# Optimization experiments

Measured on AMD Instinct MI355X. Metric: run time of the kernel, lower is better.

Reference implementation:

```python
import jax, jax.numpy as jnp
import numpy as np

N, E, G = 30000, 240000, 1000
F, H = 78, 10            # in-features, GAT heads
HID = F * H              # 780
NEG_SLOPE = 0.2


def setup_inputs() -> dict:
    key = jax.random.key(0)
    ks = jax.random.split(key, 12)
    x = jax.random.normal(ks[0], (N, F), dtype=jnp.float32)
    edge_index = jax.random.randint(ks[1], (2, E), 0, N, dtype=jnp.int32)
    batch = jnp.sort(jax.random.randint(ks[2], (N,), 0, G, dtype=jnp.int32))
    def lin(k, fan_in, shape):
        return (jax.random.normal(k, shape, dtype=jnp.float32)
                / jnp.sqrt(jnp.float32(fan_in)))
    return {
        "x": x,
        "edge_index": edge_index,
        "batch": batch,
        "W_gat": lin(ks[3], F, (F, HID)),          # GATConv lin weight
        "att_src": lin(ks[4], F, (H, F)),          # GAT attention vectors
        "att_dst": lin(ks[5], F, (H, F)),
        "b_gat": jnp.zeros((HID,), jnp.float32),
        "W_gcn": lin(ks[6], HID, (HID, HID)),
        "b_gcn": jnp.zeros((HID,), jnp.float32),
        "W1": lin(ks[7], 2 * HID, (2 * HID, 1500)),
        "b1": jnp.zeros((1500,), jnp.float32),
        "W2": lin(ks[8], 1500, (1500, 128)),
        "b2": jnp.zeros((128,), jnp.float32),
    }


def _with_self_loops(edge_index):
    loop = jnp.arange(N, dtype=edge_index.dtype)
    src = jnp.concatenate([edge_index[0], loop])
    dst = jnp.concatenate([edge_index[1], loop])
    return src, dst


def reference(x, edge_index, batch, W_gat, att_src, att_dst, b_gat,
              W_gcn, b_gcn, W1, b1, W2, b2):
    src, dst = _with_self_loops(edge_index)  # [E+N]

    # ---- GATConv(78 -> 78, heads=10, concat) ----
    h = (x @ W_gat).reshape(N, H, F)                       # [N,H,F]
    a_src = jnp.einsum('nhf,hf->nh', h, att_src)           # [N,H]
    a_dst = jnp.einsum('nhf,hf->nh', h, att_dst)
    e = jax.nn.leaky_relu(a_src[src] + a_dst[dst], NEG_SLOPE)  # [Et,H]
    # segment softmax over incoming edges of each dst node
    e_max = jax.ops.segment_max(e, dst, num_segments=N)
    e_exp = jnp.exp(e - e_max[dst])
    denom = jax.ops.segment_sum(e_exp, dst, num_segments=N)
    alpha = e_exp / denom[dst]                             # [Et,H]
    msg = h[src] * alpha[:, :, None]                       # [Et,H,F]
    out = jax.ops.segment_sum(msg, dst, num_segments=N).reshape(N, HID) + b_gat
    out = jax.nn.relu(out)

    # ---- GCNConv(780 -> 780), symmetric norm with self loops ----
    h2 = out @ W_gcn                                       # [N,HID]
    deg = jax.ops.segment_sum(jnp.ones_like(dst, jnp.float32), dst,
                              num_segments=N)
    dinv = jax.lax.rsqrt(jnp.maximum(deg, 1.0))
    norm = dinv[src] * dinv[dst]                           # [Et]
    out2 = jax.ops.segment_sum(norm[:, None] * h2[src], dst,
                               num_segments=N) + b_gcn
    out2 = jax.nn.relu(out2)

    # ---- global mean / max pool over molecules ----
    counts = jax.ops.segment_sum(jnp.ones((N,), jnp.float32), batch,
                                 num_segments=G)
    gsum = jax.ops.segment_sum(out2, batch, num_segments=G)
    gmean = gsum / jnp.maximum(counts, 1.0)[:, None]
    gmax = jax.ops.segment_max(out2, batch, num_segments=G)
    gmax = jnp.where(counts[:, None] > 0, gmax, 0.0)
    pooled = jnp.concatenate([gmean, gmax], axis=1)        # [G, 1560]

    # ---- MLP head (dropout = identity at eval) ----
    hidfc = jax.nn.relu(pooled @ W1 + b1)
    return hidfc @ W2 + b2                                 # [G, 128]
```

## Files before the change

kernel.cpp:

```cpp
#include <hip/hip_runtime.h>

#define NN 30000
#define EE 240000
#define ET 270000
#define GG 1000
#define NH 10
#define FF 78
#define HID 780
#define NEG_SLOPE 0.2f

#define LD_H 784
#define KP_GCN 800
#define NP_HID 896
#define KP_X 96
#define MP_N 30080
#define KP_P 1568
#define NP_W1 1536
#define LD_FC 1504
#define MP_G 1024

#define MT 128
#define NT 128
#define KB 32
#define GCH 16
#define NBLK 30

typedef __bf16 bf16_8 __attribute__((ext_vector_type(8)));
typedef float f32x4 __attribute__((ext_vector_type(4)));

__device__ __forceinline__ void async_copy16(const void* g, void* l) {
  __builtin_amdgcn_global_load_lds(
      (const __attribute__((address_space(1))) void*)g,
      (__attribute__((address_space(3))) void*)l, 16, 0, 0);
}

__device__ __forceinline__ float bf2f(unsigned int bits) {
  return __uint_as_float(bits << 16);
}

__global__ void init_kernel(int* __restrict__ cnt, int* __restrict__ fill,
                            int* __restrict__ lo, int* __restrict__ hi) {
  int i = blockIdx.x * blockDim.x + threadIdx.x;
  if (i < NN) { cnt[i] = 0; fill[i] = 0; }
  if (i < GG) { lo[i] = NN; hi[i] = 0; }
}

template <bool OUT_BF>
__global__ __launch_bounds__(256) void mfma_gemm(
    const __bf16* __restrict__ A, const __bf16* __restrict__ BT,
    float* __restrict__ Cf, __bf16* __restrict__ Cb,
    const float* __restrict__ bias, int M, int Kp, int Nout, int ldc,
    int relu) {
  __shared__ __bf16 As[MT][KB];
  __shared__ __bf16 Bs[NT][KB];
  int tid = threadIdx.x;
  int lane = tid & 63, wave = tid >> 6;
  int row0 = blockIdx.y * MT, col0 = blockIdx.x * NT;
  int wm = (wave & 1) * 64, wn = (wave >> 1) * 64;
  int l15 = lane & 15, quad = lane >> 4;
  f32x4 acc[4][4] = {};

  for (int k0 = 0; k0 < Kp; k0 += KB) {
    for (int t = 0; t < 2; t++) {
      int c = tid + t * 256;
      int r = c >> 2, kc = c & 3;
      const __bf16* g = A + (size_t)(row0 + r) * Kp + k0 + kc * 8;
      char* l = (char*)&As[0][0] + (size_t)((tid & ~63) + t * 256) * 16;
      async_copy16(g, l);
    }
    for (int t = 0; t < 2; t++) {
      int c = tid + t * 256;
      int r = c >> 2, kc = c & 3;
      const __bf16* g = BT + (size_t)(col0 + r) * Kp + k0 + kc * 8;
      char* l = (char*)&Bs[0][0] + (size_t)((tid & ~63) + t * 256) * 16;
      async_copy16(g, l);
    }
    __syncthreads();

    bf16_8 af[4], bfv[4];
    for (int mt = 0; mt < 4; mt++)
      af[mt] = *(const bf16_8*)&As[wm + mt * 16 + l15][quad * 8];
    for (int nt = 0; nt < 4; nt++)
      bfv[nt] = *(const bf16_8*)&Bs[wn + nt * 16 + l15][quad * 8];
    for (int mt = 0; mt < 4; mt++)
      for (int nt = 0; nt < 4; nt++)
        acc[mt][nt] = __builtin_amdgcn_mfma_f32_16x16x32_bf16(
            af[mt], bfv[nt], acc[mt][nt], 0, 0, 0);
    __syncthreads();
  }

  for (int nt = 0; nt < 4; nt++) {
    int col = col0 + wn + nt * 16 + l15;
    if (col >= ldc) continue;
    bool valid = col < Nout;
    float bv = (valid && bias) ? bias[col] : 0.f;
    for (int mt = 0; mt < 4; mt++) {
      int rbase = row0 + wm + mt * 16 + quad * 4;
      for (int r = 0; r < 4; r++) {
        int row = rbase + r;
        if (row >= M) continue;
        float v = 0.f;
        if (valid) {
          v = acc[mt][nt][r] + bv;
          if (relu) v = fmaxf(v, 0.f);
        }
        if (OUT_BF) Cb[(size_t)row * ldc + col] = (__bf16)v;
        else        Cf[(size_t)row * ldc + col] = v;
      }
    }
  }
}

__global__ void wconvT_kernel(const float* __restrict__ W,
                              __bf16* __restrict__ BT, int K, int N, int Kp,
                              int Np) {
  int i = blockIdx.x * blockDim.x + threadIdx.x;
  if (i >= Np * Kp) return;
  int n = i / Kp, k = i - n * Kp;
  BT[i] = (__bf16)((n < N && k < K) ? W[(size_t)k * N + n] : 0.f);
}

__global__ void xconv_kernel(const float* __restrict__ x,
                             __bf16* __restrict__ xb) {
  int i = blockIdx.x * blockDim.x + threadIdx.x;
  if (i >= MP_N * KP_X) return;
  int n = i / KP_X, k = i - n * KP_X;
  xb[i] = (__bf16)((n < NN && k < FF) ? x[(size_t)n * FF + k] : 0.f);
}

__global__ void wsd_kernel(const float* __restrict__ W_gat,
                           const float* __restrict__ att_src,
                           const float* __restrict__ att_dst,
                           float* __restrict__ wsd) {
  int i = blockIdx.x * blockDim.x + threadIdx.x;
  if (i >= FF * 2 * NH) return;
  int k = i / (2 * NH), c = i - k * (2 * NH);
  int h = (c < NH) ? c : c - NH;
  const float* att = (c < NH) ? att_src : att_dst;
  float s = 0.f;
  for (int f = 0; f < FF; f++)
    s += W_gat[(size_t)k * HID + h * FF + f] * att[h * FF + f];
  wsd[k * 2 * NH + c] = s;
}

__global__ __launch_bounds__(256) void adot_kernel(
    const float* __restrict__ x, const float* __restrict__ wsd,
    float* __restrict__ a_src, float* __restrict__ a_dst) {
  __shared__ float w_s[FF * 2 * NH];
  for (int i = threadIdx.x; i < FF * 2 * NH; i += 256) w_s[i] = wsd[i];
  __syncthreads();
  int gid = blockIdx.x * 256 + threadIdx.x;
  if (gid >= NN * 2 * NH) return;
  int n = gid / (2 * NH), c = gid - n * (2 * NH);
  float s = 0.f;
  for (int k = 0; k < FF; k++) s += x[(size_t)n * FF + k] * w_s[k * 2 * NH + c];
  if (c < NH) a_src[n * NH + c] = s;
  else        a_dst[n * NH + (c - NH)] = s;
}

__device__ __forceinline__ void edge_sd(const int* __restrict__ ei, int t,
                                        int& s, int& d) {
  if (t < EE) { s = ei[t]; d = ei[EE + t]; }
  else        { s = t - EE; d = t - EE; }
}

__global__ void count_kernel(const int* __restrict__ ei, int* __restrict__ cnt) {
  int t = blockIdx.x * blockDim.x + threadIdx.x;
  if (t < ET) { int s, d; edge_sd(ei, t, s, d); atomicAdd(&cnt[d], 1); }
}

__global__ __launch_bounds__(1024) void scan1_kernel(
    const int* __restrict__ cnt, int* __restrict__ row_ptr,
    int* __restrict__ partial) {
  __shared__ int buf[1024];
  int i = blockIdx.x * 1024 + threadIdx.x;
  int v = (i < NN) ? cnt[i] : 0;
  buf[threadIdx.x] = v;
  __syncthreads();
  for (int off = 1; off < 1024; off <<= 1) {
    int t = (threadIdx.x >= off) ? buf[threadIdx.x - off] : 0;
    __syncthreads();
    buf[threadIdx.x] += t;
    __syncthreads();
  }
  if (i < NN) row_ptr[i] = buf[threadIdx.x] - v;
  if (threadIdx.x == 1023) partial[blockIdx.x] = buf[1023];
}

__global__ void scan2_kernel(int* __restrict__ partial,
                             int* __restrict__ offs) {
  if (threadIdx.x == 0) {
    int run = 0;
    for (int b = 0; b < NBLK; b++) { offs[b] = run; run += partial[b]; }
  }
}

__global__ void scan3_kernel(int* __restrict__ row_ptr,
                             const int* __restrict__ offs) {
  int i = blockIdx.x * blockDim.x + threadIdx.x;
  if (i < NN) row_ptr[i] += offs[i >> 10];
  if (i == 0) row_ptr[NN] = ET;
}

__global__ void scatter_kernel(const int* __restrict__ ei,
                               const int* __restrict__ row_ptr,
                               int* __restrict__ fill,
                               const float* __restrict__ a_src,
                               const float* __restrict__ a_dst,
                               int* __restrict__ col_src,
                               float* __restrict__ p_csr) {
  int t = blockIdx.x * blockDim.x + threadIdx.x;
  if (t >= ET) return;
  int s, d; edge_sd(ei, t, s, d);
  int pos = row_ptr[d] + atomicAdd(&fill[d], 1);
  col_src[pos] = s;
#pragma unroll
  for (int h = 0; h < NH; h++) {
    float v = a_src[s * NH + h] + a_dst[d * NH + h];
    v = (v > 0.f) ? v : v * NEG_SLOPE;
    p_csr[(size_t)pos * NH + h] = __expf(v);
  }
}

__global__ void isum_kernel(const int* __restrict__ row_ptr,
                            const float* __restrict__ p_csr,
                            float* __restrict__ inv_sums) {
  int t = blockIdx.x * blockDim.x + threadIdx.x;
  if (t >= NN * NH) return;
  int d = t / NH, h = t - d * NH;
  int beg = row_ptr[d], end = row_ptr[d + 1];
  float s = 0.f;
  for (int e = beg; e < end; e++) s += p_csr[(size_t)e * NH + h];
  inv_sums[t] = 1.f / s;
}

__global__ void dinv_kernel(const int* __restrict__ row_ptr,
                            float* __restrict__ dinv) {
  int i = blockIdx.x * blockDim.x + threadIdx.x;
  if (i < NN) {
    int d = row_ptr[i + 1] - row_ptr[i];
    dinv[i] = rsqrtf((float)max(d, 1));
  }
}

__global__ __launch_bounds__(128) void gat_aggr_kernel(
    const int* __restrict__ row_ptr, const int* __restrict__ col_src,
    const float* __restrict__ p_csr, const float* __restrict__ inv_sums,
    const __bf16* __restrict__ h_bf, const float* __restrict__ b_gat,
    __bf16* __restrict__ A_bf) {
  int d = blockIdx.x;
  int beg = row_ptr[d], end = row_ptr[d + 1];
  int tid = threadIdx.x;
  __shared__ float inv_s[NH];
  __shared__ float al_s[GCH][NH];
  __shared__ int src_s[GCH];
  if (tid < NH) inv_s[tid] = inv_sums[d * NH + tid];
  __syncthreads();

  int f0 = 8 * tid;
  int h0 = f0 / FF; if (h0 > NH - 1) h0 = NH - 1;
  int split = (h0 + 1) * FF - f0; if (split > 8) split = 8;
  int h1 = (h0 < NH - 1) ? h0 + 1 : NH - 1;
  float acc[8] = {};

  for (int c = beg; c < end; c += GCH) {
    int ce = min(GCH, end - c);
    if (tid < ce) src_s[tid] = col_src[c + tid];
    for (int i = tid; i < ce * NH; i += 128) {
      int j = i / NH, h = i - j * NH;
      al_s[j][h] = p_csr[(size_t)(c + j) * NH + h] * inv_s[h];
    }
    __syncthreads();
    if (tid < 98) {
      for (int j = 0; j < ce; j++) {
        uint4 r = *(const uint4*)(h_bf + (size_t)src_s[j] * LD_H + f0);
        float a0 = al_s[j][h0], a1 = al_s[j][h1];
        unsigned int w[4] = {r.x, r.y, r.z, r.w};
#pragma unroll
        for (int k = 0; k < 8; k++) {
          unsigned int bits = (k & 1) ? (w[k >> 1] >> 16) : (w[k >> 1] & 0xffffu);
          acc[k] += bf2f(bits) * ((k < split) ? a0 : a1);
        }
      }
    }
    __syncthreads();
  }
  if (tid < 100) {
    bf16_8 ov;
#pragma unroll
    for (int k = 0; k < 8; k++) {
      int f = f0 + k;
      float val = 0.f;
      if (tid < 98 && f < HID) val = fmaxf(acc[k] + b_gat[f], 0.f);
      ov[k] = (__bf16)val;
    }
    *(bf16_8*)(A_bf + (size_t)d * KP_GCN + f0) = ov;
  }
}

__global__ __launch_bounds__(128) void gcn_aggr_kernel(
    const int* __restrict__ row_ptr, const int* __restrict__ col_src,
    const float* __restrict__ dinv, const __bf16* __restrict__ h2,
    const float* __restrict__ b_gcn, __bf16* __restrict__ out2) {
  int d = blockIdx.x;
  int beg = row_ptr[d], end = row_ptr[d + 1];
  int tid = threadIdx.x;
  float dv = dinv[d];
  __shared__ float w_s[GCH];
  __shared__ int src_s[GCH];
  int f0 = 8 * tid;
  float acc[8] = {};
  for (int c = beg; c < end; c += GCH) {
    int ce = min(GCH, end - c);
    if (tid < ce) {
      int s = col_src[c + tid];
      src_s[tid] = s;
      w_s[tid] = dinv[s] * dv;
    }
    __syncthreads();
    if (tid < 98) {
      for (int j = 0; j < ce; j++) {
        uint4 r = *(const uint4*)(h2 + (size_t)src_s[j] * LD_H + f0);
        float w = w_s[j];
        unsigned int wb[4] = {r.x, r.y, r.z, r.w};
#pragma unroll
        for (int k = 0; k < 8; k++) {
          unsigned int bits = (k & 1) ? (wb[k >> 1] >> 16) : (wb[k >> 1] & 0xffffu);
          acc[k] += bf2f(bits) * w;
        }
      }
    }
    __syncthreads();
  }
  if (tid < 98) {
    bf16_8 ov;
#pragma unroll
    for (int k = 0; k < 8; k++) {
      int f = f0 + k;
      float val = (f < HID) ? fmaxf(acc[k] + b_gcn[f], 0.f) : 0.f;
      ov[k] = (__bf16)val;
    }
    *(bf16_8*)(out2 + (size_t)d * LD_H + f0) = ov;
  }
}

__global__ void bounds_kernel(const int* __restrict__ batch,
                              int* __restrict__ lo, int* __restrict__ hi) {
  int i = blockIdx.x * blockDim.x + threadIdx.x;
  if (i < NN) {
    int g = batch[i];
    atomicMin(&lo[g], i);
    atomicMax(&hi[g], i + 1);
  }
}

__global__ __launch_bounds__(832) void pool_kernel(
    const __bf16* __restrict__ out2, const int* __restrict__ lo,
    const int* __restrict__ hi, __bf16* __restrict__ pooled) {
  int g = blockIdx.x;
  int l = lo[g], h = hi[g];
  int f = threadIdx.x;
  if (f >= HID) {
    int pad = f - HID;
    if (pad < KP_P - 2 * HID)
      pooled[(size_t)g * KP_P + 2 * HID + pad] = (__bf16)0.f;
    return;
  }
  float s = 0.f, mx = -1e30f;
  for (int n = l; n < h; n++) {
    float v = (float)out2[(size_t)n * LD_H + f];
    s += v;
    mx = fmaxf(mx, v);
  }
  if (h <= l) { s = 0.f; mx = 0.f; }
  else s = s / (float)(h - l);
  pooled[(size_t)g * KP_P + f] = (__bf16)s;
  pooled[(size_t)g * KP_P + HID + f] = (__bf16)mx;
}

extern "C" void kernel_launch(void* const* d_in, const int* in_sizes, int n_in,
                              void* d_out, int out_size, void* d_ws,
                              size_t ws_size, hipStream_t stream) {
  const float* x        = (const float*)d_in[0];
  const int*   edge_idx = (const int*)d_in[1];
  const int*   batch    = (const int*)d_in[2];
  const float* W_gat    = (const float*)d_in[3];
  const float* att_src  = (const float*)d_in[4];
  const float* att_dst  = (const float*)d_in[5];
  const float* b_gat    = (const float*)d_in[6];
  const float* W_gcn    = (const float*)d_in[7];
  const float* b_gcn    = (const float*)d_in[8];
  const float* W1       = (const float*)d_in[9];
  const float* b1       = (const float*)d_in[10];
  const float* W2       = (const float*)d_in[11];
  const float* b2       = (const float*)d_in[12];
  float* out = (float*)d_out;
  (void)in_sizes; (void)n_in; (void)out_size; (void)ws_size;

  char* ws = (char*)d_ws;
  size_t off = 0;
  auto alloc = [&](size_t bytes) -> void* {
    void* p = ws + off;
    off += (bytes + 255) & ~(size_t)255;
    return p;
  };
  char*  bufR     = (char*)alloc((size_t)MP_N * KP_GCN * 2);
  __bf16* A_bf    = (__bf16*)bufR;
  __bf16* out2b   = (__bf16*)bufR;
  __bf16* h_bf    = (__bf16*)alloc((size_t)MP_N * LD_H * 2);
  __bf16* h2_bf   = (__bf16*)alloc((size_t)MP_N * LD_H * 2);
  __bf16* x_bf    = (__bf16*)alloc((size_t)MP_N * KP_X * 2);
  __bf16* WgatT   = (__bf16*)alloc((size_t)NP_HID * KP_X * 2);
  __bf16* WgcnT   = (__bf16*)alloc((size_t)NP_HID * KP_GCN * 2);
  __bf16* W1T     = (__bf16*)alloc((size_t)NP_W1 * KP_P * 2);
  __bf16* W2T     = (__bf16*)alloc((size_t)128 * LD_FC * 2);
  __bf16* pooled  = (__bf16*)alloc((size_t)MP_G * KP_P * 2);
  __bf16* hidfc   = (__bf16*)alloc((size_t)MP_G * LD_FC * 2);
  float* wsd      = (float*)alloc((size_t)FF * 2 * NH * 4);
  float* a_src_b  = (float*)alloc((size_t)NN * NH * 4);
  float* a_dst_b  = (float*)alloc((size_t)NN * NH * 4);
  float* p_csr    = (float*)alloc((size_t)ET * NH * 4);
  float* inv_sums = (float*)alloc((size_t)NN * NH * 4);
  int*   cnt      = (int*)alloc((size_t)NN * 4);
  int*   fill     = (int*)alloc((size_t)NN * 4);
  int*   row_ptr  = (int*)alloc((size_t)(NN + 1) * 4);
  int*   col_src  = (int*)alloc((size_t)ET * 4);
  int*   partial  = (int*)alloc((size_t)NBLK * 4);
  int*   offs     = (int*)alloc((size_t)NBLK * 4);
  int*   lo       = (int*)alloc((size_t)GG * 4);
  int*   hi       = (int*)alloc((size_t)GG * 4);
  float* dinv     = (float*)alloc((size_t)NN * 4);

  init_kernel<<<(NN + 255) / 256, 256, 0, stream>>>(cnt, fill, lo, hi);

  xconv_kernel<<<(MP_N * KP_X + 255) / 256, 256, 0, stream>>>(x, x_bf);
  wconvT_kernel<<<(NP_HID * KP_X + 255) / 256, 256, 0, stream>>>(
      W_gat, WgatT, FF, HID, KP_X, NP_HID);
  wconvT_kernel<<<(NP_HID * KP_GCN + 255) / 256, 256, 0, stream>>>(
      W_gcn, WgcnT, HID, HID, KP_GCN, NP_HID);
  wconvT_kernel<<<(NP_W1 * KP_P + 255) / 256, 256, 0, stream>>>(
      W1, W1T, 2 * HID, 1500, KP_P, NP_W1);
  wconvT_kernel<<<(128 * LD_FC + 255) / 256, 256, 0, stream>>>(
      W2, W2T, 1500, 128, LD_FC, 128);
  wsd_kernel<<<(FF * 2 * NH + 255) / 256, 256, 0, stream>>>(
      W_gat, att_src, att_dst, wsd);

  {
    dim3 grid(NP_HID / NT, MP_N / MT);
    mfma_gemm<true><<<grid, 256, 0, stream>>>(x_bf, WgatT, nullptr, h_bf,
                                              nullptr, NN, KP_X, HID, LD_H, 0);
  }
  adot_kernel<<<(NN * 2 * NH + 255) / 256, 256, 0, stream>>>(x, wsd, a_src_b,
                                                             a_dst_b);

  count_kernel<<<(ET + 255) / 256, 256, 0, stream>>>(edge_idx, cnt);
  scan1_kernel<<<NBLK, 1024, 0, stream>>>(cnt, row_ptr, partial);
  scan2_kernel<<<1, 64, 0, stream>>>(partial, offs);
  scan3_kernel<<<(NN + 255) / 256, 256, 0, stream>>>(row_ptr, offs);
  scatter_kernel<<<(ET + 255) / 256, 256, 0, stream>>>(
      edge_idx, row_ptr, fill, a_src_b, a_dst_b, col_src, p_csr);
  isum_kernel<<<(NN * NH + 255) / 256, 256, 0, stream>>>(row_ptr, p_csr,
                                                         inv_sums);
  dinv_kernel<<<(NN + 255) / 256, 256, 0, stream>>>(row_ptr, dinv);

  gat_aggr_kernel<<<NN, 128, 0, stream>>>(row_ptr, col_src, p_csr, inv_sums,
                                          h_bf, b_gat, A_bf);
  {
    dim3 grid(NP_HID / NT, MP_N / MT);
    mfma_gemm<true><<<grid, 256, 0, stream>>>(A_bf, WgcnT, nullptr, h2_bf,
                                              nullptr, NN, KP_GCN, HID, LD_H, 0);
  }
  gcn_aggr_kernel<<<NN, 128, 0, stream>>>(row_ptr, col_src, dinv, h2_bf,
                                          b_gcn, out2b);

  bounds_kernel<<<(NN + 255) / 256, 256, 0, stream>>>(batch, lo, hi);
  pool_kernel<<<GG, 832, 0, stream>>>(out2b, lo, hi, pooled);

  {
    dim3 grid(NP_W1 / NT, MP_G / MT);
    mfma_gemm<true><<<grid, 256, 0, stream>>>(pooled, W1T, nullptr, hidfc, b1,
                                              GG, KP_P, 1500, LD_FC, 1);
  }
  {
    dim3 grid(1, MP_G / MT);
    mfma_gemm<false><<<grid, 256, 0, stream>>>(hidfc, W2T, out, nullptr, b2,
                                               GG, LD_FC, 128, 128, 0);
  }
}
```

Baseline: 617.2 us.

## Fuse small preprocessing kernels, k-major LDS layout and XCD-aware GCN GEMM tiling

Several changes at once. The GEMM shared-memory tiles move to a k-chunk-major layout, which changes the LDS read pattern and targets bank conflicts. The GCN GEMM gets a remapped 1D grid that groups row tiles by blockIdx mod 8, presumably for per-XCD L2 reuse. The softmax denominator kernel is removed and the sums are built inside the GAT aggregation with shared atomics. The dinv and batch-bounds kernels are folded into scan3 and count. These cut launch count and an extra pass over p_csr, at the cost of LDS atomics in the aggregation loop.

Result: no change. 612.1 us (-0.8%).

```diff
diff --git a/kernel.cpp b/kernel.cpp
--- a/kernel.cpp
+++ b/kernel.cpp
@@ -50,38 +50,51 @@
     const __bf16* __restrict__ A, const __bf16* __restrict__ BT,
     float* __restrict__ Cf, __bf16* __restrict__ Cb,
     const float* __restrict__ bias, int M, int Kp, int Nout, int ldc,
-    int relu) {
-  __shared__ __bf16 As[MT][KB];
-  __shared__ __bf16 Bs[NT][KB];
+    int relu, int rp, int nct, int mtiles) {
+  __shared__ __bf16 As[4][MT][8];
+  __shared__ __bf16 Bs[4][NT][8];
+  int rt, ct;
+  if (rp > 0) {
+    int bid = blockIdx.x;
+    int p = bid & 7, s = bid >> 3;
+    int q = s / nct;
+    rt = p * rp + q;
+    ct = s - q * nct;
+    if (rt >= mtiles) return;
+  } else {
+    rt = blockIdx.y; ct = blockIdx.x;
+  }
+  int row0 = rt * MT, col0 = ct * NT;
   int tid = threadIdx.x;
   int lane = tid & 63, wave = tid >> 6;
-  int row0 = blockIdx.y * MT, col0 = blockIdx.x * NT;
   int wm = (wave & 1) * 64, wn = (wave >> 1) * 64;
   int l15 = lane & 15, quad = lane >> 4;
   f32x4 acc[4][4] = {};
 
   for (int k0 = 0; k0 < Kp; k0 += KB) {
     for (int t = 0; t < 2; t++) {
-      int c = tid + t * 256;
-      int r = c >> 2, kc = c & 3;
+      int base = t * 256 + wave * 64;
+      int s = base + lane;
+      int kc = s >> 7, r = s & 127;
       const __bf16* g = A + (size_t)(row0 + r) * Kp + k0 + kc * 8;
-      char* l = (char*)&As[0][0] + (size_t)((tid & ~63) + t * 256) * 16;
+      char* l = (char*)&As[0][0][0] + (size_t)base * 16;
       async_copy16(g, l);
     }
     for (int t = 0; t < 2; t++) {
-      int c = tid + t * 256;
-      int r = c >> 2, kc = c & 3;
+      int base = t * 256 + wave * 64;
+      int s = base + lane;
+      int kc = s >> 7, r = s & 127;
       const __bf16* g = BT + (size_t)(col0 + r) * Kp + k0 + kc * 8;
-      char* l = (char*)&Bs[0][0] + (size_t)((tid & ~63) + t * 256) * 16;
+      char* l = (char*)&Bs[0][0][0] + (size_t)base * 16;
       async_copy16(g, l);
     }
     __syncthreads();
 
     bf16_8 af[4], bfv[4];
     for (int mt = 0; mt < 4; mt++)
-      af[mt] = *(const bf16_8*)&As[wm + mt * 16 + l15][quad * 8];
+      af[mt] = *(const bf16_8*)&As[quad][wm + mt * 16 + l15][0];
     for (int nt = 0; nt < 4; nt++)
-      bfv[nt] = *(const bf16_8*)&Bs[wn + nt * 16 + l15][quad * 8];
+      bfv[nt] = *(const bf16_8*)&Bs[quad][wn + nt * 16 + l15][0];
     for (int mt = 0; mt < 4; mt++)
       for (int nt = 0; nt < 4; nt++)
         acc[mt][nt] = __builtin_amdgcn_mfma_f32_16x16x32_bf16(
@@ -164,9 +177,17 @@
   else        { s = t - EE; d = t - EE; }
 }
 
-__global__ void count_kernel(const int* __restrict__ ei, int* __restrict__ cnt) {
+__global__ void count_kernel(const int* __restrict__ ei,
+                             const int* __restrict__ batch,
+                             int* __restrict__ cnt, int* __restrict__ lo,
+                             int* __restrict__ hi) {
   int t = blockIdx.x * blockDim.x + threadIdx.x;
   if (t < ET) { int s, d; edge_sd(ei, t, s, d); atomicAdd(&cnt[d], 1); }
+  if (t < NN) {
+    int g = batch[t];
+    atomicMin(&lo[g], t);
+    atomicMax(&hi[g], t + 1);
+  }
 }
 
 __global__ __launch_bounds__(1024) void scan1_kernel(
@@ -196,9 +217,14 @@
 }
 
 __global__ void scan3_kernel(int* __restrict__ row_ptr,
-                             const int* __restrict__ offs) {
+                             const int* __restrict__ offs,
+                             const int* __restrict__ cnt,
+                             float* __restrict__ dinv) {
   int i = blockIdx.x * blockDim.x + threadIdx.x;
-  if (i < NN) row_ptr[i] += offs[i >> 10];
+  if (i < NN) {
+    row_ptr[i] += offs[i >> 10];
+    dinv[i] = rsqrtf((float)max(cnt[i], 1));
+  }
   if (i == 0) row_ptr[NN] = ET;
 }
 
@@ -222,39 +248,17 @@
   }
 }
 
-__global__ void isum_kernel(const int* __restrict__ row_ptr,
-                            const float* __restrict__ p_csr,
-                            float* __restrict__ inv_sums) {
-  int t = blockIdx.x * blockDim.x + threadIdx.x;
-  if (t >= NN * NH) return;
-  int d = t / NH, h = t - d * NH;
-  int beg = row_ptr[d], end = row_ptr[d + 1];
-  float s = 0.f;
-  for (int e = beg; e < end; e++) s += p_csr[(size_t)e * NH + h];
-  inv_sums[t] = 1.f / s;
-}
-
-__global__ void dinv_kernel(const int* __restrict__ row_ptr,
-                            float* __restrict__ dinv) {
-  int i = blockIdx.x * blockDim.x + threadIdx.x;
-  if (i < NN) {
-    int d = row_ptr[i + 1] - row_ptr[i];
-    dinv[i] = rsqrtf((float)max(d, 1));
-  }
-}
-
 __global__ __launch_bounds__(128) void gat_aggr_kernel(
     const int* __restrict__ row_ptr, const int* __restrict__ col_src,
-    const float* __restrict__ p_csr, const float* __restrict__ inv_sums,
-    const __bf16* __restrict__ h_bf, const float* __restrict__ b_gat,
-    __bf16* __restrict__ A_bf) {
+    const float* __restrict__ p_csr, const __bf16* __restrict__ h_bf,
+    const float* __restrict__ b_gat, __bf16* __restrict__ A_bf) {
   int d = blockIdx.x;
   int beg = row_ptr[d], end = row_ptr[d + 1];
   int tid = threadIdx.x;
-  __shared__ float inv_s[NH];
+  __shared__ float sum_s[NH];
   __shared__ float al_s[GCH][NH];
   __shared__ int src_s[GCH];
-  if (tid < NH) inv_s[tid] = inv_sums[d * NH + tid];
+  if (tid < NH) sum_s[tid] = 0.f;
   __syncthreads();
 
   int f0 = 8 * tid;
@@ -268,7 +272,9 @@
     if (tid < ce) src_s[tid] = col_src[c + tid];
     for (int i = tid; i < ce * NH; i += 128) {
       int j = i / NH, h = i - j * NH;
-      al_s[j][h] = p_csr[(size_t)(c + j) * NH + h] * inv_s[h];
+      float p = p_csr[(size_t)(c + j) * NH + h];
+      al_s[j][h] = p;
+      atomicAdd(&sum_s[h], p);
     }
     __syncthreads();
     if (tid < 98) {
@@ -286,12 +292,15 @@
     __syncthreads();
   }
   if (tid < 100) {
+    float inv0 = 0.f, inv1 = 0.f;
+    if (tid < 98) { inv0 = 1.f / sum_s[h0]; inv1 = 1.f / sum_s[h1]; }
     bf16_8 ov;
 #pragma unroll
     for (int k = 0; k < 8; k++) {
       int f = f0 + k;
       float val = 0.f;
-      if (tid < 98 && f < HID) val = fmaxf(acc[k] + b_gat[f], 0.f);
+      if (tid < 98 && f < HID)
+        val = fmaxf(acc[k] * ((k < split) ? inv0 : inv1) + b_gat[f], 0.f);
       ov[k] = (__bf16)val;
     }
     *(bf16_8*)(A_bf + (size_t)d * KP_GCN + f0) = ov;
@@ -341,16 +350,6 @@
       ov[k] = (__bf16)val;
     }
     *(bf16_8*)(out2 + (size_t)d * LD_H + f0) = ov;
-  }
-}
-
-__global__ void bounds_kernel(const int* __restrict__ batch,
-                              int* __restrict__ lo, int* __restrict__ hi) {
-  int i = blockIdx.x * blockDim.x + threadIdx.x;
-  if (i < NN) {
-    int g = batch[i];
-    atomicMin(&lo[g], i);
-    atomicMax(&hi[g], i + 1);
   }
 }
 
@@ -420,7 +419,6 @@
   float* a_src_b  = (float*)alloc((size_t)NN * NH * 4);
   float* a_dst_b  = (float*)alloc((size_t)NN * NH * 4);
   float* p_csr    = (float*)alloc((size_t)ET * NH * 4);
-  float* inv_sums = (float*)alloc((size_t)NN * NH * 4);
   int*   cnt      = (int*)alloc((size_t)NN * 4);
   int*   fill     = (int*)alloc((size_t)NN * 4);
   int*   row_ptr  = (int*)alloc((size_t)(NN + 1) * 4);
@@ -448,42 +446,42 @@
   {
     dim3 grid(NP_HID / NT, MP_N / MT);
     mfma_gemm<true><<<grid, 256, 0, stream>>>(x_bf, WgatT, nullptr, h_bf,
-                                              nullptr, NN, KP_X, HID, LD_H, 0);
+                                              nullptr, NN, KP_X, HID, LD_H, 0,
+                                              0, 0, 0);
   }
   adot_kernel<<<(NN * 2 * NH + 255) / 256, 256, 0, stream>>>(x, wsd, a_src_b,
                                                              a_dst_b);
 
-  count_kernel<<<(ET + 255) / 256, 256, 0, stream>>>(edge_idx, cnt);
+  count_kernel<<<(ET + 255) / 256, 256, 0, stream>>>(edge_idx, batch, cnt, lo,
+                                                     hi);
   scan1_kernel<<<NBLK, 1024, 0, stream>>>(cnt, row_ptr, partial);
   scan2_kernel<<<1, 64, 0, stream>>>(partial, offs);
-  scan3_kernel<<<(NN + 255) / 256, 256, 0, stream>>>(row_ptr, offs);
+  scan3_kernel<<<(NN + 255) / 256, 256, 0, stream>>>(row_ptr, offs, cnt, dinv);
   scatter_kernel<<<(ET + 255) / 256, 256, 0, stream>>>(
       edge_idx, row_ptr, fill, a_src_b, a_dst_b, col_src, p_csr);
-  isum_kernel<<<(NN * NH + 255) / 256, 256, 0, stream>>>(row_ptr, p_csr,
-                                                         inv_sums);
-  dinv_kernel<<<(NN + 255) / 256, 256, 0, stream>>>(row_ptr, dinv);
-
-  gat_aggr_kernel<<<NN, 128, 0, stream>>>(row_ptr, col_src, p_csr, inv_sums,
-                                          h_bf, b_gat, A_bf);
+
+  gat_aggr_kernel<<<NN, 128, 0, stream>>>(row_ptr, col_src, p_csr, h_bf,
+                                          b_gat, A_bf);
   {
-    dim3 grid(NP_HID / NT, MP_N / MT);
-    mfma_gemm<true><<<grid, 256, 0, stream>>>(A_bf, WgcnT, nullptr, h2_bf,
-                                              nullptr, NN, KP_GCN, HID, LD_H, 0);
+    mfma_gemm<true><<<dim3(8 * 30 * 7), 256, 0, stream>>>(
+        A_bf, WgcnT, nullptr, h2_bf, nullptr, NN, KP_GCN, HID, LD_H, 0,
+        30, 7, MP_N / MT);
   }
   gcn_aggr_kernel<<<NN, 128, 0, stream>>>(row_ptr, col_src, dinv, h2_bf,
                                           b_gcn, out2b);
 
-  bounds_kernel<<<(NN + 255) / 256, 256, 0, stream>>>(batch, lo, hi);
   pool_kernel<<<GG, 832, 0, stream>>>(out2b, lo, hi, pooled);
 
   {
     dim3 grid(NP_W1 / NT, MP_G / MT);
     mfma_gemm<true><<<grid, 256, 0, stream>>>(pooled, W1T, nullptr, hidfc, b1,
-                                              GG, KP_P, 1500, LD_FC, 1);
+                                              GG, KP_P, 1500, LD_FC, 1,
+                                              0, 0, 0);
   }
   {
     dim3 grid(1, MP_G / MT);
     mfma_gemm<false><<<grid, 256, 0, stream>>>(hidfc, W2T, out, nullptr, b2,
-                                               GG, LD_FC, 128, 128, 0);
-  }
-}
+                                               GG, LD_FC, 128, 128, 0,
+                                               0, 0, 0);
+  }
+}
```
